# Performance work log

Hardware: AMD Instinct MI355X
Metric: run time of the kernel (lower is better)

Reference implementation:

```python
import jax, jax.numpy as jnp
import numpy as np

P = 16          # patch size
NH = 12         # num heads
DH = 64         # head dim
C = 768         # embed dim
DEPTH = 12
HID = 3072      # mlp hidden = 4*C
EPS = 1e-6


def _ln(x, g, b):
    m = x.mean(-1, keepdims=True)
    v = ((x - m) ** 2).mean(-1, keepdims=True)
    return (x - m) / jnp.sqrt(v + EPS) * g + b


def _rope_tables(seq_len, dim):
    inv_freq = 1.0 / (10000.0 ** (jnp.arange(0, dim, 2, dtype=jnp.float32) / dim))
    freqs = jnp.arange(seq_len, dtype=jnp.float32)[:, None] * inv_freq[None, :]  # [S, dim/2]
    emb = jnp.concatenate([freqs, freqs], axis=-1)  # [S, dim] (concat layout, as in source)
    return jnp.cos(emb), jnp.sin(emb)


def _apply_rope(q, k, cos, sin):
    def rot(t):  # interleaved rotate-half, exactly as torch source
        t1, t2 = t[..., ::2], t[..., 1::2]
        return jnp.stack([-t2, t1], axis=-1).reshape(t.shape)
    return q * cos + rot(q) * sin, k * cos + rot(k) * sin


def setup_inputs() -> dict:
    key = jax.random.key(0)
    ks = jax.random.split(key, 16)
    w = lambda k, shp: (jax.random.normal(k, shp, dtype=jnp.float32) * 0.02)
    inp = {
        "x": jax.random.normal(ks[0], (4, 6, 320, 320), dtype=jnp.float32),
        "conv_w": w(ks[1], (C, 3, P, P)),
        "conv_b": jnp.zeros((C,), jnp.float32),
        "ln1_g": jnp.ones((DEPTH, C), jnp.float32),
        "ln1_b": jnp.zeros((DEPTH, C), jnp.float32),
        "qkv_w": w(ks[2], (DEPTH, C, 3 * C)),
        "qkv_b": jnp.zeros((DEPTH, 3 * C), jnp.float32),
        "proj_w": w(ks[3], (DEPTH, C, C)),
        "proj_b": jnp.zeros((DEPTH, C), jnp.float32),
        "ln2_g": jnp.ones((DEPTH, C), jnp.float32),
        "ln2_b": jnp.zeros((DEPTH, C), jnp.float32),
        "fc1_w": w(ks[4], (DEPTH, C, HID)),
        "fc1_b": jnp.zeros((DEPTH, HID), jnp.float32),
        "fc2_w": w(ks[5], (DEPTH, HID, C)),
        "fc2_b": jnp.zeros((DEPTH, C), jnp.float32),
        "lnf_g": jnp.ones((C,), jnp.float32),
        "lnf_b": jnp.zeros((C,), jnp.float32),
    }
    return inp


def reference(x, conv_w, conv_b, ln1_g, ln1_b, qkv_w, qkv_b, proj_w, proj_b,
              ln2_g, ln2_b, fc1_w, fc1_b, fc2_w, fc2_b, lnf_g, lnf_b):
    B = x.shape[0]

    def embed(img):  # [B,3,H,W] -> [B, (H/P)*(W/P), C]
        y = jax.lax.conv_general_dilated(
            img, conv_w, window_strides=(P, P), padding="VALID",
            dimension_numbers=("NCHW", "OIHW", "NCHW")) + conv_b[None, :, None, None]
        b, c, hg, wg = y.shape
        return y.reshape(b, c, hg * wg).transpose(0, 2, 1)

    t = jnp.concatenate([embed(x[:, :3]), embed(x[:, 3:])], axis=1)  # [B,S,C], S=2*400=800
    S = t.shape[1]
    cos, sin = _rope_tables(S, DH)
    cos, sin = cos[None, None], sin[None, None]  # [1,1,S,DH]
    scale = DH ** -0.5

    def block(h, p):
        l1g, l1b, qw, qb, pw, pb, l2g, l2b, f1w, f1b, f2w, f2b = p
        y = _ln(h, l1g, l1b)
        qkv = (y @ qw + qb).reshape(B, S, 3, NH, DH).transpose(2, 0, 3, 1, 4)
        q, k, v = qkv[0], qkv[1], qkv[2]  # [B,NH,S,DH]
        q, k = _apply_rope(q, k, cos, sin)
        a = jax.nn.softmax(jnp.einsum("bhsd,bhtd->bhst", q, k) * scale, axis=-1)
        o = jnp.einsum("bhst,bhtd->bhsd", a, v).transpose(0, 2, 1, 3).reshape(B, S, C)
        h = h + (o @ pw + pb)
        y = _ln(h, l2g, l2b)
        h = h + (jax.nn.gelu(y @ f1w + f1b, approximate=False) @ f2w + f2b)
        return h, None

    params = (ln1_g, ln1_b, qkv_w, qkv_b, proj_w, proj_b,
              ln2_g, ln2_b, fc1_w, fc1_b, fc2_w, fc2_b)
    t, _ = jax.lax.scan(block, t, params)
    return _ln(t, lnf_g, lnf_b)
```

## Files before the change

kernel.cpp:

```cpp
#include <hip/hip_runtime.h>
#include <hip/hip_bf16.h>
#include <math.h>

#define S_LEN   800
#define SP_LEN  896
#define C_DIM   768
#define NHEAD   12
#define DHEAD   64
#define HID_DIM 3072
#define BATCH   4
#define NTOK    (BATCH * S_LEN)
#define DEPTH_N 12

using bf16x8 = __attribute__((ext_vector_type(8))) short;
using f32x4  = __attribute__((ext_vector_type(4))) float;

__device__ inline short f2bf(float x) {
    unsigned u = __builtin_bit_cast(unsigned, x);
    u += 0x7fff + ((u >> 16) & 1);
    return (short)(u >> 16);
}
__device__ inline float bf2f(short x) {
    unsigned u = ((unsigned)(unsigned short)x) << 16;
    return __builtin_bit_cast(float, u);
}

typedef const __attribute__((address_space(1))) void* gas_ptr;
typedef __attribute__((address_space(3))) void* las_ptr;
__device__ inline void async_copy16(const void* g, void* l) {
    __builtin_amdgcn_global_load_lds((gas_ptr)g, (las_ptr)l, 16, 0, 0);
}

__device__ inline int xcd_remap(int bid, int nwg) {
    int x = bid & 7, q = nwg >> 3, r = nwg & 7;
    int base = (x < r) ? x * (q + 1) : r * (q + 1) + (x - r) * q;
    return base + (bid >> 3);
}

struct TP4 {
    const float *qw, *pw, *f1, *f2;
    short *wq, *wp, *w1, *w2;
};

template <int K, int N>
__device__ __forceinline__ void tc_tile(const float* __restrict__ W,
                                        short* __restrict__ Wt, int t) {
    __shared__ float tile[32][33];
    int nb = t % (N / 32), kb = t / (N / 32);
    int k0 = kb * 32, n0 = nb * 32;
    int tx = threadIdx.x & 31, ty = threadIdx.x >> 5;
#pragma unroll
    for (int i = ty; i < 32; i += 8)
        tile[i][tx] = W[(size_t)(k0 + i) * N + n0 + tx];
    __syncthreads();
#pragma unroll
    for (int i = ty; i < 32; i += 8)
        Wt[(size_t)(n0 + i) * K + k0 + tx] = f2bf(tile[tx][i]);
}

__global__ __launch_bounds__(256)
void transpose4_kernel(TP4 p) {
    int t = blockIdx.x;
    if (t < 1728)          tc_tile<768, 2304>(p.qw, p.wq, t);
    else if (t < 2304)     tc_tile<768, 768>(p.pw, p.wp, t - 1728);
    else if (t < 4608)     tc_tile<768, 3072>(p.f1, p.w1, t - 2304);
    else                   tc_tile<3072, 768>(p.f2, p.w2, t - 4608);
}

__global__ void convert_bf_kernel(const float* __restrict__ a, short* __restrict__ o, int n) {
    int i = blockIdx.x * 256 + threadIdx.x;
    if (i < n) o[i] = f2bf(a[i]);
}

__global__ void im2col_kernel(const float* __restrict__ x, short* __restrict__ A) {
    int idx = blockIdx.x * 256 + threadIdx.x;
    if (idx >= NTOK * 768) return;
    int kk = idx % 768;
    int s  = (idx / 768) % S_LEN;
    int b  = idx / (768 * S_LEN);
    int c  = kk / 256;
    int i  = (kk / 16) % 16;
    int j  = kk % 16;
    int half = s / 400, ss = s % 400;
    int hg = ss / 20, wg = ss % 20;
    int ch = half * 3 + c;
    A[idx] = f2bf(x[((size_t)(b * 6 + ch) * 320 + hg * 16 + i) * 320 + wg * 16 + j]);
}

template <int BN, bool GELU, bool RES, bool OBF>
__global__ __launch_bounds__(256)
void gemm_mfma(const short* __restrict__ A, const short* __restrict__ Bt,
               const float* __restrict__ bias, const float* __restrict__ res,
               void* __restrict__ Cout, int M, int N, int K) {
    constexpr int BM = 128, BK = 64;
    constexpr int TI = (BN == 128) ? 4 : 2;
    constexpr int TJ = 4;
    constexpr int ACALLS = BM * BK / (8 * 64);
    constexpr int BCALLS = BN * BK / (8 * 64);

    __shared__ __align__(16) short As[BM * BK];
    __shared__ __align__(16) short Bs[BN * BK];

    int tid = threadIdx.x;
    int w = tid >> 6, lane = tid & 63;

    int nwg = gridDim.x * gridDim.y;
    int flat = xcd_remap(blockIdx.x + gridDim.x * blockIdx.y, nwg);
    int bx = flat % gridDim.x, by = flat / gridDim.x;
    int m0 = by * BM, n0 = bx * BN;

    int wr = (BN == 128) ? (w >> 1) * 64 : w * 32;
    int wc = (BN == 128) ? (w & 1) * 64 : 0;

    f32x4 acc[TI][TJ];
#pragma unroll
    for (int i = 0; i < TI; ++i)
#pragma unroll
        for (int j = 0; j < TJ; ++j)
            acc[i][j] = (f32x4){0.f, 0.f, 0.f, 0.f};

    int lc = lane & 15, lq = lane >> 4;

    for (int k0 = 0; k0 < K; k0 += BK) {
#pragma unroll
        for (int j = w; j < ACALLS; j += 4) {
            int c = j * 64 + lane;
            int row = c >> 3, p = c & 7, q = p ^ (row & 7);
            async_copy16(A + (size_t)(m0 + row) * K + k0 + q * 8, As + j * 512);
        }
#pragma unroll
        for (int j = w; j < BCALLS; j += 4) {
            int c = j * 64 + lane;
            int row = c >> 3, p = c & 7, q = p ^ (row & 7);
            async_copy16(Bt + (size_t)(n0 + row) * K + k0 + q * 8, Bs + j * 512);
        }
        __syncthreads();

#pragma unroll
        for (int h = 0; h < 2; ++h) {
            bf16x8 afrag[TI], bfrag[TJ];
#pragma unroll
            for (int i = 0; i < TI; ++i) {
                int row = wr + i * 16 + lc;
                afrag[i] = *(const bf16x8*)(As + row * 64 + ((((h << 2) | lq)) ^ (row & 7)) * 8);
            }
#pragma unroll
            for (int j = 0; j < TJ; ++j) {
                int col = wc + j * 16 + lc;
                bfrag[j] = *(const bf16x8*)(Bs + col * 64 + ((((h << 2) | lq)) ^ (col & 7)) * 8);
            }
#pragma unroll
            for (int i = 0; i < TI; ++i)
#pragma unroll
                for (int j = 0; j < TJ; ++j)
                    acc[i][j] = __builtin_amdgcn_mfma_f32_16x16x32_bf16(
                        afrag[i], bfrag[j], acc[i][j], 0, 0, 0);
        }
        __syncthreads();
    }

    int rbase = lq * 4;
#pragma unroll
    for (int i = 0; i < TI; ++i)
#pragma unroll
        for (int j = 0; j < TJ; ++j)
#pragma unroll
            for (int r = 0; r < 4; ++r) {
                int m = m0 + wr + i * 16 + rbase + r;
                int n = n0 + wc + j * 16 + lc;
                float v = acc[i][j][r] + bias[n];
                if (RES) v += res[(size_t)m * N + n];
                if (GELU) v = 0.5f * v * (1.0f + erff(v * 0.70710678118654752f));
                if (OBF) ((short*)Cout)[(size_t)m * N + n] = f2bf(v);
                else     ((float*)Cout)[(size_t)m * N + n] = v;
            }
}

template <bool OBF>
__global__ __launch_bounds__(256)
void ln_kernel(const float* __restrict__ x, const float* __restrict__ g,
               const float* __restrict__ bta, void* __restrict__ yv) {
    int row = blockIdx.x;
    const float* xr = x + (size_t)row * C_DIM;
    int tid = threadIdx.x;

    float v0 = xr[tid], v1 = xr[tid + 256], v2 = xr[tid + 512];
    float s  = v0 + v1 + v2;
    float sq = v0 * v0 + v1 * v1 + v2 * v2;
#pragma unroll
    for (int off = 32; off; off >>= 1) {
        s  += __shfl_down(s, off);
        sq += __shfl_down(sq, off);
    }
    __shared__ float red1[4], red2[4];
    __shared__ float mean_s, rstd_s;
    int wv = tid / 64, lane = tid % 64;
    if (lane == 0) { red1[wv] = s; red2[wv] = sq; }
    __syncthreads();
    if (tid == 0) {
        float S1 = red1[0] + red1[1] + red1[2] + red1[3];
        float S2 = red2[0] + red2[1] + red2[2] + red2[3];
        float m = S1 / (float)C_DIM;
        float var = S2 / (float)C_DIM - m * m;
        mean_s = m;
        rstd_s = rsqrtf(var + 1e-6f);
    }
    __syncthreads();
    float m = mean_s, r = rstd_s;
    float o0 = (v0 - m) * r * g[tid]       + bta[tid];
    float o1 = (v1 - m) * r * g[tid + 256] + bta[tid + 256];
    float o2 = (v2 - m) * r * g[tid + 512] + bta[tid + 512];
    if (OBF) {
        short* yr = (short*)yv + (size_t)row * C_DIM;
        yr[tid] = f2bf(o0); yr[tid + 256] = f2bf(o1); yr[tid + 512] = f2bf(o2);
    } else {
        float* yr = (float*)yv + (size_t)row * C_DIM;
        yr[tid] = o0; yr[tid + 256] = o1; yr[tid + 512] = o2;
    }
}

__global__ __launch_bounds__(256)
void rope_qkv_kernel(const short* __restrict__ qkv, short* __restrict__ qb,
                     short* __restrict__ kb, short* __restrict__ vtb) {
    int bh = blockIdx.x;
    int st = blockIdx.y;
    int b = bh / NHEAD, h = bh % NHEAD;
    int s0 = st * 64;

    __shared__ __align__(16) short vlds[64][72];

    int tid = threadIdx.x;
    int sl = tid >> 2;
    int dc = (tid & 3) * 16;
    int s = s0 + sl;

    short qo[16], ko[16];
    if (s < S_LEN) {
        const short* base = qkv + ((size_t)(b * S_LEN + s)) * (3 * C_DIM) + h * DHEAD + dc;
        short qsh[16], ksh[16], vsh[16];
        *(bf16x8*)(qsh)     = *(const bf16x8*)(base);
        *(bf16x8*)(qsh + 8) = *(const bf16x8*)(base + 8);
        *(bf16x8*)(ksh)     = *(const bf16x8*)(base + C_DIM);
        *(bf16x8*)(ksh + 8) = *(const bf16x8*)(base + C_DIM + 8);
        *(bf16x8*)(vsh)     = *(const bf16x8*)(base + 2 * C_DIM);
        *(bf16x8*)(vsh + 8) = *(const bf16x8*)(base + 2 * C_DIM + 8);
        float qv[16], kv[16];
#pragma unroll
        for (int i = 0; i < 16; ++i) { qv[i] = bf2f(qsh[i]); kv[i] = bf2f(ksh[i]); }
#pragma unroll
        for (int i = 0; i < 16; ++i) {
            int d = dc + i;
            float ang = (float)s * exp2f(-(float)(d & 31) * 0.41524101186092029f);
            float c = cosf(ang), sn = sinf(ang);
            float sign = (i & 1) ? 1.0f : -1.0f;
            qo[i] = f2bf((qv[i] * c + sign * qv[i ^ 1] * sn) * 0.18033688011112042f);
            ko[i] = f2bf(kv[i] * c + sign * kv[i ^ 1] * sn);
        }
        *(bf16x8*)&vlds[sl][dc]     = *(bf16x8*)(vsh);
        *(bf16x8*)&vlds[sl][dc + 8] = *(bf16x8*)(vsh + 8);
    } else {
#pragma unroll
        for (int i = 0; i < 16; ++i) { qo[i] = 0; ko[i] = 0; vlds[sl][dc + i] = 0; }
    }
    {
        short* qd = qb + ((size_t)bh * SP_LEN + s) * DHEAD + dc;
        short* kd = kb + ((size_t)bh * SP_LEN + s) * DHEAD + dc;
        *(bf16x8*)(qd)     = *(bf16x8*)(qo);
        *(bf16x8*)(qd + 8) = *(bf16x8*)(qo + 8);
        *(bf16x8*)(kd)     = *(bf16x8*)(ko);
        *(bf16x8*)(kd + 8) = *(bf16x8*)(ko + 8);
    }
    __syncthreads();
    {
        int dr = tid >> 2, sc = (tid & 3) * 16;
        short vo[16];
#pragma unroll
        for (int i = 0; i < 16; ++i) vo[i] = vlds[sc + i][dr];
        short* vd = vtb + ((size_t)bh * DHEAD + dr) * SP_LEN + s0 + sc;
        *(bf16x8*)(vd)     = *(bf16x8*)(vo);
        *(bf16x8*)(vd + 8) = *(bf16x8*)(vo + 8);
    }
}

__global__ __launch_bounds__(256)
void attn_mfma_kernel(const short* __restrict__ qb, const short* __restrict__ kb,
                      const short* __restrict__ vtb, short* __restrict__ o) {
    int bh = blockIdx.x;
    int qt = blockIdx.y;
    int b = bh / NHEAD, h = bh % NHEAD;
    int m0 = qt * 64;

    __shared__ __align__(16) short Qs[64 * 64];
    __shared__ __align__(16) short Ks[128 * 64];
    __shared__ __align__(16) short Vts[64 * 128];
    __shared__ __align__(16) short Ps[64 * 136];

    int tid = threadIdx.x;
    int w = tid >> 6, lane = tid & 63;
    int lc = lane & 15, lq = lane >> 4;
    int kq = lq * 8;

    const short* qbase = qb + (size_t)bh * SP_LEN * DHEAD;
    const short* kbase = kb + (size_t)bh * SP_LEN * DHEAD;
    const short* vbase = vtb + (size_t)bh * DHEAD * SP_LEN;

    f32x4 oacc[4];
#pragma unroll
    for (int t = 0; t < 4; ++t) oacc[t] = (f32x4){0.f, 0.f, 0.f, 0.f};
    float mrow[4] = {-3.0e38f, -3.0e38f, -3.0e38f, -3.0e38f};
    float lrow[4] = {0.f, 0.f, 0.f, 0.f};

#pragma unroll
    for (int j = w; j < 8; j += 4) {
        int c = j * 64 + lane;
        int row = c >> 3, p = c & 7, q = p ^ (row & 7);
        async_copy16(qbase + (size_t)(m0 + row) * DHEAD + q * 8, Qs + j * 512);
    }

    bf16x8 aq0, aq1;

    for (int it = 0; it < 7; ++it) {
        int kt = it * 128;
#pragma unroll
        for (int j = w; j < 16; j += 4) {
            int c = j * 64 + lane;
            int row = c >> 3, p = c & 7, q = p ^ (row & 7);
            async_copy16(kbase + (size_t)(kt + row) * DHEAD + q * 8, Ks + j * 512);
        }
#pragma unroll
        for (int j = w; j < 16; j += 4) {
            int c = j * 64 + lane;
            int d = c >> 4, p = c & 15, sq = p ^ (d & 15);
            async_copy16(vbase + (size_t)d * SP_LEN + kt + sq * 8, Vts + j * 512);
        }
        __syncthreads();

        int nt = (it < 6) ? 8 : 2;

        if (it == 0) {
            int qrow = w * 16 + lc;
            aq0 = *(const bf16x8*)(Qs + qrow * 64 + ((lq) ^ (qrow & 7)) * 8);
            aq1 = *(const bf16x8*)(Qs + qrow * 64 + ((4 | lq) ^ (qrow & 7)) * 8);
        }

        f32x4 sacc[8];
        __builtin_amdgcn_s_setprio(1);
        for (int t = 0; t < nt; ++t) {
            int kr = t * 16 + lc;
            bf16x8 bk0 = *(const bf16x8*)(Ks + kr * 64 + ((lq) ^ (kr & 7)) * 8);
            bf16x8 bk1 = *(const bf16x8*)(Ks + kr * 64 + ((4 | lq) ^ (kr & 7)) * 8);
            f32x4 z = (f32x4){0.f, 0.f, 0.f, 0.f};
            z = __builtin_amdgcn_mfma_f32_16x16x32_bf16(aq0, bk0, z, 0, 0, 0);
            z = __builtin_amdgcn_mfma_f32_16x16x32_bf16(aq1, bk1, z, 0, 0, 0);
            sacc[t] = z;
        }
        __builtin_amdgcn_s_setprio(0);

        float rmax[4];
#pragma unroll
        for (int r = 0; r < 4; ++r) {
            float m = sacc[0][r];
            for (int t = 1; t < nt; ++t) m = fmaxf(m, sacc[t][r]);
            rmax[r] = m;
        }
#pragma unroll
        for (int off = 1; off < 16; off <<= 1)
#pragma unroll
            for (int r = 0; r < 4; ++r)
                rmax[r] = fmaxf(rmax[r], __shfl_xor(rmax[r], off));

        float alpha[4], rsum[4] = {0.f, 0.f, 0.f, 0.f};
#pragma unroll
        for (int r = 0; r < 4; ++r) {
            float mnew = fmaxf(mrow[r], rmax[r]);
            alpha[r] = exp2f(mrow[r] - mnew);
            mrow[r] = mnew;
        }
        for (int t = 0; t < nt; ++t) {
#pragma unroll
            for (int r = 0; r < 4; ++r) {
                float p = exp2f(sacc[t][r] - mrow[r]);
                rsum[r] += p;
                Ps[(w * 16 + lq * 4 + r) * 136 + t * 16 + lc] = f2bf(p);
            }
        }
#pragma unroll
        for (int off = 1; off < 16; off <<= 1)
#pragma unroll
            for (int r = 0; r < 4; ++r)
                rsum[r] += __shfl_xor(rsum[r], off);
#pragma unroll
        for (int r = 0; r < 4; ++r) lrow[r] = lrow[r] * alpha[r] + rsum[r];
#pragma unroll
        for (int t = 0; t < 4; ++t)
#pragma unroll
            for (int r = 0; r < 4; ++r) oacc[t][r] *= alpha[r];

        int nk = (nt == 8) ? 4 : 1;
        __builtin_amdgcn_s_setprio(1);
        for (int kstep = 0; kstep < nk; ++kstep) {
            bf16x8 ap = *(const bf16x8*)(Ps + (w * 16 + lc) * 136 + kstep * 32 + kq);
#pragma unroll
            for (int t = 0; t < 4; ++t) {
                int dr = t * 16 + lc;
                bf16x8 bv = *(const bf16x8*)(Vts + dr * 128 + ((((kstep << 2) | lq)) ^ (dr & 15)) * 8);
                oacc[t] = __builtin_amdgcn_mfma_f32_16x16x32_bf16(ap, bv, oacc[t], 0, 0, 0);
            }
        }
        __builtin_amdgcn_s_setprio(0);
        __syncthreads();
    }

    float inv_l[4];
#pragma unroll
    for (int r = 0; r < 4; ++r) inv_l[r] = 1.0f / lrow[r];
#pragma unroll
    for (int t = 0; t < 4; ++t)
#pragma unroll
        for (int r = 0; r < 4; ++r) {
            int row = w * 16 + lq * 4 + r;
            int s = m0 + row;
            if (s < S_LEN) {
                int n = t * 16 + lc;
                o[((size_t)(b * S_LEN + s)) * C_DIM + h * DHEAD + n] = f2bf(oacc[t][r] * inv_l[r]);
            }
        }
}

extern "C" void kernel_launch(void* const* d_in, const int* in_sizes, int n_in,
                              void* d_out, int out_size, void* d_ws, size_t ws_size,
                              hipStream_t stream) {
    const float* x      = (const float*)d_in[0];
    const float* conv_w = (const float*)d_in[1];
    const float* conv_b = (const float*)d_in[2];
    const float* ln1_g  = (const float*)d_in[3];
    const float* ln1_b  = (const float*)d_in[4];
    const float* qkv_w  = (const float*)d_in[5];
    const float* qkv_b  = (const float*)d_in[6];
    const float* proj_w = (const float*)d_in[7];
    const float* proj_b = (const float*)d_in[8];
    const float* ln2_g  = (const float*)d_in[9];
    const float* ln2_b  = (const float*)d_in[10];
    const float* fc1_w  = (const float*)d_in[11];
    const float* fc1_b  = (const float*)d_in[12];
    const float* fc2_w  = (const float*)d_in[13];
    const float* fc2_b  = (const float*)d_in[14];
    const float* lnf_g  = (const float*)d_in[15];
    const float* lnf_b  = (const float*)d_in[16];

    const size_t NTC = (size_t)NTOK * C_DIM;
    const size_t HSD = (size_t)BATCH * NHEAD * SP_LEN * DHEAD;
    float* ws = (float*)d_ws;
    float* h       = ws;
    short* qkv_bf  = (short*)(h + NTC);
    short* qb      = qkv_bf + (size_t)NTOK * 3 * C_DIM;
    short* kb      = qb + HSD;
    short* vtb     = kb + HSD;
    short* y_bf    = vtb + HSD;
    short* big_bf  = y_bf + NTC;
    short* wq      = big_bf + (size_t)NTOK * HID_DIM;
    short* wp      = wq + (size_t)3 * C_DIM * C_DIM;
    short* w1      = wp + (size_t)C_DIM * C_DIM;
    short* w2      = w1 + (size_t)C_DIM * HID_DIM;
    short* embed_wt = w2 + (size_t)HID_DIM * C_DIM;

    convert_bf_kernel<<<(768 * 768 + 255) / 256, 256, 0, stream>>>(conv_w, embed_wt, 768 * 768);
    im2col_kernel<<<(NTOK * 768 + 255) / 256, 256, 0, stream>>>(x, big_bf);
    gemm_mfma<64, false, false, false><<<dim3(C_DIM / 64, NTOK / 128), 256, 0, stream>>>(
        big_bf, embed_wt, conv_b, nullptr, h, NTOK, C_DIM, C_DIM);

    for (int l = 0; l < DEPTH_N; ++l) {
        const float* l1g = ln1_g + (size_t)l * C_DIM;
        const float* l1b = ln1_b + (size_t)l * C_DIM;
        const float* qw  = qkv_w + (size_t)l * C_DIM * 3 * C_DIM;
        const float* qbs = qkv_b + (size_t)l * 3 * C_DIM;
        const float* pw  = proj_w + (size_t)l * C_DIM * C_DIM;
        const float* pb  = proj_b + (size_t)l * C_DIM;
        const float* l2g = ln2_g + (size_t)l * C_DIM;
        const float* l2b = ln2_b + (size_t)l * C_DIM;
        const float* f1w = fc1_w + (size_t)l * C_DIM * HID_DIM;
        const float* f1b = fc1_b + (size_t)l * HID_DIM;
        const float* f2w = fc2_w + (size_t)l * HID_DIM * C_DIM;
        const float* f2b = fc2_b + (size_t)l * C_DIM;

        TP4 tp{qw, pw, f1w, f2w, wq, wp, w1, w2};
        transpose4_kernel<<<6912, 256, 0, stream>>>(tp);

        ln_kernel<true><<<NTOK, 256, 0, stream>>>(h, l1g, l1b, y_bf);
        gemm_mfma<128, false, false, true><<<dim3(3 * C_DIM / 128, NTOK / 128), 256, 0, stream>>>(
            y_bf, wq, qbs, nullptr, qkv_bf, NTOK, 3 * C_DIM, C_DIM);

        rope_qkv_kernel<<<dim3(BATCH * NHEAD, 14), 256, 0, stream>>>(qkv_bf, qb, kb, vtb);
        attn_mfma_kernel<<<dim3(BATCH * NHEAD, 13), 256, 0, stream>>>(qb, kb, vtb, y_bf);

        gemm_mfma<64, false, true, false><<<dim3(C_DIM / 64, NTOK / 128), 256, 0, stream>>>(
            y_bf, wp, pb, h, h, NTOK, C_DIM, C_DIM);

        ln_kernel<true><<<NTOK, 256, 0, stream>>>(h, l2g, l2b, y_bf);
        gemm_mfma<128, true, false, true><<<dim3(HID_DIM / 128, NTOK / 128), 256, 0, stream>>>(
            y_bf, w1, f1b, nullptr, big_bf, NTOK, HID_DIM, C_DIM);
        gemm_mfma<64, false, true, false><<<dim3(C_DIM / 64, NTOK / 128), 256, 0, stream>>>(
            big_bf, w2, f2b, h, h, NTOK, C_DIM, HID_DIM);
    }

    ln_kernel<false><<<NTOK, 256, 0, stream>>>(h, lnf_g, lnf_b, d_out);
}
```

Measured before the change: 2.645 ms.

## Batch all-layer weight transposes into one launch and transpose S tile in attention

```diff
diff --git a/kernel.cpp b/kernel.cpp
--- a/kernel.cpp
+++ b/kernel.cpp
@@ -13,6 +13,7 @@
 #define DEPTH_N 12
 
 using bf16x8 = __attribute__((ext_vector_type(8))) short;
+using bf16x4 = __attribute__((ext_vector_type(4))) short;
 using f32x4  = __attribute__((ext_vector_type(4))) float;
 
 __device__ inline short f2bf(float x) {
@@ -36,11 +37,6 @@
     int base = (x < r) ? x * (q + 1) : r * (q + 1) + (x - r) * q;
     return base + (bid >> 3);
 }
-
-struct TP4 {
-    const float *qw, *pw, *f1, *f2;
-    short *wq, *wp, *w1, *w2;
-};
 
 template <int K, int N>
 __device__ __forceinline__ void tc_tile(const float* __restrict__ W,
@@ -59,12 +55,20 @@
 }
 
 __global__ __launch_bounds__(256)
-void transpose4_kernel(TP4 p) {
+void transpose_all_kernel(const float* __restrict__ qkv_w, const float* __restrict__ proj_w,
+                          const float* __restrict__ fc1_w, const float* __restrict__ fc2_w,
+                          short* __restrict__ wq, short* __restrict__ wp,
+                          short* __restrict__ w1, short* __restrict__ w2) {
     int t = blockIdx.x;
-    if (t < 1728)          tc_tile<768, 2304>(p.qw, p.wq, t);
-    else if (t < 2304)     tc_tile<768, 768>(p.pw, p.wp, t - 1728);
-    else if (t < 4608)     tc_tile<768, 3072>(p.f1, p.w1, t - 2304);
-    else                   tc_tile<3072, 768>(p.f2, p.w2, t - 4608);
+    int l = t / 6912, u = t % 6912;
+    if (u < 1728)
+        tc_tile<768, 2304>(qkv_w + (size_t)l * 768 * 2304, wq + (size_t)l * 2304 * 768, u);
+    else if (u < 2304)
+        tc_tile<768, 768>(proj_w + (size_t)l * 768 * 768, wp + (size_t)l * 768 * 768, u - 1728);
+    else if (u < 4608)
+        tc_tile<768, 3072>(fc1_w + (size_t)l * 768 * 3072, w1 + (size_t)l * 3072 * 768, u - 2304);
+    else
+        tc_tile<3072, 768>(fc2_w + (size_t)l * 3072 * 768, w2 + (size_t)l * 768 * 3072, u - 4608);
 }
 
 __global__ void convert_bf_kernel(const float* __restrict__ a, short* __restrict__ o, int n) {
@@ -307,8 +311,8 @@
     f32x4 oacc[4];
 #pragma unroll
     for (int t = 0; t < 4; ++t) oacc[t] = (f32x4){0.f, 0.f, 0.f, 0.f};
-    float mrow[4] = {-3.0e38f, -3.0e38f, -3.0e38f, -3.0e38f};
-    float lrow[4] = {0.f, 0.f, 0.f, 0.f};
+    float mrow = -3.0e38f;
+    float lrow = 0.f;
 
 #pragma unroll
     for (int j = w; j < 8; j += 4) {
@@ -350,51 +354,45 @@
             bf16x8 bk0 = *(const bf16x8*)(Ks + kr * 64 + ((lq) ^ (kr & 7)) * 8);
             bf16x8 bk1 = *(const bf16x8*)(Ks + kr * 64 + ((4 | lq) ^ (kr & 7)) * 8);
             f32x4 z = (f32x4){0.f, 0.f, 0.f, 0.f};
-            z = __builtin_amdgcn_mfma_f32_16x16x32_bf16(aq0, bk0, z, 0, 0, 0);
-            z = __builtin_amdgcn_mfma_f32_16x16x32_bf16(aq1, bk1, z, 0, 0, 0);
+            z = __builtin_amdgcn_mfma_f32_16x16x32_bf16(bk0, aq0, z, 0, 0, 0);
+            z = __builtin_amdgcn_mfma_f32_16x16x32_bf16(bk1, aq1, z, 0, 0, 0);
             sacc[t] = z;
         }
         __builtin_amdgcn_s_setprio(0);
 
-        float rmax[4];
+        float rmx = sacc[0][0];
+#pragma unroll
+        for (int t = 0; t < nt; ++t)
+#pragma unroll
+            for (int r = 0; r < 4; ++r) rmx = fmaxf(rmx, sacc[t][r]);
+        rmx = fmaxf(rmx, __shfl_xor(rmx, 16));
+        rmx = fmaxf(rmx, __shfl_xor(rmx, 32));
+
+        float mnew = fmaxf(mrow, rmx);
+        float alpha = exp2f(mrow - mnew);
+        mrow = mnew;
+
+        float rsum = 0.f;
+        for (int t = 0; t < nt; ++t) {
+            bf16x4 pk;
+#pragma unroll
+            for (int r = 0; r < 4; ++r) {
+                float p = exp2f(sacc[t][r] - mrow);
+                rsum += p;
+                pk[r] = f2bf(p);
+            }
+            *(bf16x4*)(Ps + (w * 16 + lc) * 136 + t * 16 + lq * 4) = pk;
+        }
+        rsum += __shfl_xor(rsum, 16);
+        rsum += __shfl_xor(rsum, 32);
+        lrow = lrow * alpha + rsum;
+
 #pragma unroll
         for (int r = 0; r < 4; ++r) {
-            float m = sacc[0][r];
-            for (int t = 1; t < nt; ++t) m = fmaxf(m, sacc[t][r]);
-            rmax[r] = m;
-        }
-#pragma unroll
-        for (int off = 1; off < 16; off <<= 1)
-#pragma unroll
-            for (int r = 0; r < 4; ++r)
-                rmax[r] = fmaxf(rmax[r], __shfl_xor(rmax[r], off));
-
-        float alpha[4], rsum[4] = {0.f, 0.f, 0.f, 0.f};
-#pragma unroll
-        for (int r = 0; r < 4; ++r) {
-            float mnew = fmaxf(mrow[r], rmax[r]);
-            alpha[r] = exp2f(mrow[r] - mnew);
-            mrow[r] = mnew;
-        }
-        for (int t = 0; t < nt; ++t) {
-#pragma unroll
-            for (int r = 0; r < 4; ++r) {
-                float p = exp2f(sacc[t][r] - mrow[r]);
-                rsum[r] += p;
-                Ps[(w * 16 + lq * 4 + r) * 136 + t * 16 + lc] = f2bf(p);
-            }
-        }
-#pragma unroll
-        for (int off = 1; off < 16; off <<= 1)
-#pragma unroll
-            for (int r = 0; r < 4; ++r)
-                rsum[r] += __shfl_xor(rsum[r], off);
-#pragma unroll
-        for (int r = 0; r < 4; ++r) lrow[r] = lrow[r] * alpha[r] + rsum[r];
-#pragma unroll
-        for (int t = 0; t < 4; ++t)
-#pragma unroll
-            for (int r = 0; r < 4; ++r) oacc[t][r] *= alpha[r];
+            float ar = __shfl(alpha, lq * 4 + r);
+#pragma unroll
+            for (int t = 0; t < 4; ++t) oacc[t][r] *= ar;
+        }
 
         int nk = (nt == 8) ? 4 : 1;
         __builtin_amdgcn_s_setprio(1);
@@ -411,9 +409,10 @@
         __syncthreads();
     }
 
+    float rl = 1.0f / lrow;
     float inv_l[4];
 #pragma unroll
-    for (int r = 0; r < 4; ++r) inv_l[r] = 1.0f / lrow[r];
+    for (int r = 0; r < 4; ++r) inv_l[r] = __shfl(rl, lq * 4 + r);
 #pragma unroll
     for (int t = 0; t < 4; ++t)
 #pragma unroll
@@ -450,6 +449,11 @@
 
     const size_t NTC = (size_t)NTOK * C_DIM;
     const size_t HSD = (size_t)BATCH * NHEAD * SP_LEN * DHEAD;
+    const size_t WQ_L = (size_t)3 * C_DIM * C_DIM;
+    const size_t WP_L = (size_t)C_DIM * C_DIM;
+    const size_t W1_L = (size_t)C_DIM * HID_DIM;
+    const size_t W2_L = (size_t)HID_DIM * C_DIM;
+
     float* ws = (float*)d_ws;
     float* h       = ws;
     short* qkv_bf  = (short*)(h + NTC);
@@ -458,13 +462,16 @@
     short* vtb     = kb + HSD;
     short* y_bf    = vtb + HSD;
     short* big_bf  = y_bf + NTC;
-    short* wq      = big_bf + (size_t)NTOK * HID_DIM;
-    short* wp      = wq + (size_t)3 * C_DIM * C_DIM;
-    short* w1      = wp + (size_t)C_DIM * C_DIM;
-    short* w2      = w1 + (size_t)C_DIM * HID_DIM;
-    short* embed_wt = w2 + (size_t)HID_DIM * C_DIM;
+    short* wq_all  = big_bf + (size_t)NTOK * HID_DIM;
+    short* wp_all  = wq_all + DEPTH_N * WQ_L;
+    short* w1_all  = wp_all + DEPTH_N * WP_L;
+    short* w2_all  = w1_all + DEPTH_N * W1_L;
+    short* embed_wt = w2_all + DEPTH_N * W2_L;
 
     convert_bf_kernel<<<(768 * 768 + 255) / 256, 256, 0, stream>>>(conv_w, embed_wt, 768 * 768);
+    transpose_all_kernel<<<DEPTH_N * 6912, 256, 0, stream>>>(
+        qkv_w, proj_w, fc1_w, fc2_w, wq_all, wp_all, w1_all, w2_all);
+
     im2col_kernel<<<(NTOK * 768 + 255) / 256, 256, 0, stream>>>(x, big_bf);
     gemm_mfma<64, false, false, false><<<dim3(C_DIM / 64, NTOK / 128), 256, 0, stream>>>(
         big_bf, embed_wt, conv_b, nullptr, h, NTOK, C_DIM, C_DIM);
@@ -472,19 +479,16 @@
     for (int l = 0; l < DEPTH_N; ++l) {
         const float* l1g = ln1_g + (size_t)l * C_DIM;
         const float* l1b = ln1_b + (size_t)l * C_DIM;
-        const float* qw  = qkv_w + (size_t)l * C_DIM * 3 * C_DIM;
         const float* qbs = qkv_b + (size_t)l * 3 * C_DIM;
-        const float* pw  = proj_w + (size_t)l * C_DIM * C_DIM;
         const float* pb  = proj_b + (size_t)l * C_DIM;
         const float* l2g = ln2_g + (size_t)l * C_DIM;
         const float* l2b = ln2_b + (size_t)l * C_DIM;
-        const float* f1w = fc1_w + (size_t)l * C_DIM * HID_DIM;
         const float* f1b = fc1_b + (size_t)l * HID_DIM;
-        const float* f2w = fc2_w + (size_t)l * HID_DIM * C_DIM;
         const float* f2b = fc2_b + (size_t)l * C_DIM;
-
-        TP4 tp{qw, pw, f1w, f2w, wq, wp, w1, w2};
-        transpose4_kernel<<<6912, 256, 0, stream>>>(tp);
+        const short* wq = wq_all + (size_t)l * WQ_L;
+        const short* wp = wp_all + (size_t)l * WP_L;
+        const short* w1 = w1_all + (size_t)l * W1_L;
+        const short* w2 = w2_all + (size_t)l * W2_L;
 
         ln_kernel<true><<<NTOK, 256, 0, stream>>>(h, l1g, l1b, y_bf);
         gemm_mfma<128, false, false, true><<<dim3(3 * C_DIM / 128, NTOK / 128), 256, 0, stream>>>(
```

New measurement: 2.645 ms. No clear change (+0.0%).
